# Optimization experiments

Measured on AMD Instinct MI355X. Metric: run time of the kernel, lower is better.

## Reference

```python
import jax, jax.numpy as jnp
import numpy as np

B, IN_DIM, MEM = 8192, 4096, 256
MIN_TS, MAX_TS, EPS = 0.1, 10.0, 1e-6
LN_EPS = 1e-5


def setup_inputs() -> dict:
    key = jax.random.key(0)
    ks = jax.random.split(key, 10)
    std = 0.02
    d_in = MEM + IN_DIM  # 4352
    return {
        "x": jax.random.normal(ks[0], (B, IN_DIM), jnp.float32),
        "h": jax.random.normal(ks[1], (B, MEM), jnp.float32),
        # memory_target: Linear(d_in, 2*MEM) -> LN -> GELU -> Linear(2*MEM, MEM)
        "W1": std * jax.random.normal(ks[2], (d_in, 2 * MEM), jnp.float32),
        "b1": jnp.zeros((2 * MEM,), jnp.float32),
        "g1": jnp.ones((2 * MEM,), jnp.float32),
        "be1": jnp.zeros((2 * MEM,), jnp.float32),
        "W2": std * jax.random.normal(ks[3], (2 * MEM, MEM), jnp.float32),
        "b2": jnp.zeros((MEM,), jnp.float32),
        # decay_gate: Linear(d_in, MEM) -> sigmoid
        "Wd": std * jax.random.normal(ks[4], (d_in, MEM), jnp.float32),
        "bd": jnp.zeros((MEM,), jnp.float32),
        # input_gate: Linear(d_in, MEM) -> sigmoid
        "Wu": std * jax.random.normal(ks[5], (d_in, MEM), jnp.float32),
        "bu": jnp.zeros((MEM,), jnp.float32),
    }


def _layernorm(t, g, b):
    mu = jnp.mean(t, axis=-1, keepdims=True)
    var = jnp.mean(jnp.square(t - mu), axis=-1, keepdims=True)
    return (t - mu) * jax.lax.rsqrt(var + LN_EPS) * g + b


def reference(x, h, W1, b1, g1, be1, W2, b2, Wd, bd, Wu, bu):
    combined = jnp.concatenate([h, x], axis=-1)  # [B, MEM+IN_DIM]
    # memory_target branch: Linear -> LayerNorm -> GELU (exact) -> Linear -> tanh
    t = _layernorm(combined @ W1 + b1, g1, be1)
    t = jax.nn.gelu(t, approximate=False)
    h_candidate = jnp.tanh(t @ W2 + b2)  # [B, MEM]
    # gates
    decay = jax.nn.sigmoid(combined @ Wd + bd)
    update = jax.nn.sigmoid(combined @ Wu + bu)
    decay = MIN_TS + (MAX_TS - MIN_TS) * decay + EPS
    new_h = (1.0 - update) * (h / decay) + update * h_candidate
    # normalize_memory: rescale new_h to old h's L2 norm
    h_norm = jnp.maximum(jnp.linalg.norm(h, axis=-1, keepdims=True), EPS)
    nh_norm = jnp.maximum(jnp.linalg.norm(new_h, axis=-1, keepdims=True), 1e-12)
    new_h = new_h / nh_norm * h_norm
    return new_h
```

## Files before the change

### kernel.cpp

```cpp
#include <hip/hip_runtime.h>
#include <stdint.h>

typedef unsigned short u16;

#define B_ROWS 8192
#define IN_DIM 4096
#define MEM 256
#define D_IN 4352
#define N1 1024
#define K2 512
#define LN_EPS 1e-5f

typedef __attribute__((ext_vector_type(4))) float f32x4;
typedef __attribute__((ext_vector_type(4))) uint32_t u32x4;
typedef __attribute__((ext_vector_type(4))) unsigned short u16x4;
typedef __attribute__((ext_vector_type(8))) short bf16x8;

#define AS1(p) ((__attribute__((address_space(1))) void*)(p))
#define AS3(p) ((__attribute__((address_space(3))) void*)(p))

__device__ __forceinline__ float bf2f(u16 u) {
  union { uint32_t u; float f; } c; c.u = ((uint32_t)u) << 16; return c.f;
}
__device__ __forceinline__ u16 f2bf(float f) {
  union { float f; uint32_t u; } c; c.f = f;
  uint32_t r = (c.u + 0x7fffu + ((c.u >> 16) & 1u)) >> 16;
  return (u16)r;
}
__device__ __forceinline__ uint32_t fbits(float f) {
  union { float f; uint32_t u; } c; c.f = f; return c.u;
}
__device__ __forceinline__ uint32_t pack_trunc(float a, float b) {
  return (fbits(b) & 0xFFFF0000u) | (fbits(a) >> 16);
}

__global__ __launch_bounds__(256)
void transpose_cast_fused(const float* __restrict__ W1, const float* __restrict__ Wd,
                          const float* __restrict__ Wu, u16* __restrict__ WT) {
  __shared__ u16 tile[64][68];
  int n0 = blockIdx.x * 64, k0 = blockIdx.y * 64;
  const float* src; int srcN, ns0;
  if (n0 < 512)      { src = W1; srcN = 512; ns0 = n0; }
  else if (n0 < 768) { src = Wd; srcN = 256; ns0 = n0 - 512; }
  else               { src = Wu; srcN = 256; ns0 = n0 - 768; }
  int t = threadIdx.x;
  int rr = t >> 4;
  int c4 = (t & 15) * 4;
#pragma unroll
  for (int i = 0; i < 4; i++) {
    int k = i * 16 + rr;
    f32x4 v = *(const f32x4*)&src[(size_t)(k0 + k) * srcN + ns0 + c4];
    tile[c4 + 0][k] = f2bf(v[0]);
    tile[c4 + 1][k] = f2bf(v[1]);
    tile[c4 + 2][k] = f2bf(v[2]);
    tile[c4 + 3][k] = f2bf(v[3]);
  }
  __syncthreads();
#pragma unroll
  for (int i = 0; i < 4; i++) {
    int n = i * 16 + rr;
    u16x4 w;
    w.x = tile[n][c4 + 0];
    w.y = tile[n][c4 + 1];
    w.z = tile[n][c4 + 2];
    w.w = tile[n][c4 + 3];
    *(u16x4*)&WT[(size_t)(n0 + n) * D_IN + k0 + c4] = w;
  }
}

__global__ void transpose_cast(const float* __restrict__ src, u16* __restrict__ dst,
                               int K, int N) {
  __shared__ u16 tile[32][34];
  int n0 = blockIdx.x * 32, k0 = blockIdx.y * 32;
  int tx = threadIdx.x, ty = threadIdx.y;
#pragma unroll
  for (int i = 0; i < 4; i++)
    tile[ty + i * 8][tx] = f2bf(src[(size_t)(k0 + ty + i * 8) * N + n0 + tx]);
  __syncthreads();
#pragma unroll
  for (int i = 0; i < 4; i++)
    dst[(size_t)(n0 + ty + i * 8) * K + k0 + tx] = tile[tx][ty + i * 8];
}

__global__ __launch_bounds__(256, 2)
void gemm1_kernel(const float* __restrict__ x, const float* __restrict__ h,
                  const u16* __restrict__ WT, u16* __restrict__ G) {
  __shared__ __attribute__((aligned(16))) u16 As[128 * 64];
  __shared__ __attribute__((aligned(16))) u16 Bs[128 * 64];
  const int t = threadIdx.x;
  const int lane = t & 63, wave = t >> 6;
  const int bx = blockIdx.x >> 6;
  const int by = blockIdx.x & 63;
  const int row0 = by * 128, col0 = bx * 128;
  const int q = lane >> 4, mrow = lane & 15;
  const int wm = wave >> 1, wn = wave & 1;

  int ar[4], ac[4];
#pragma unroll
  for (int j = 0; j < 4; j++) {
    int idx = j * 256 + t;
    int r = idx >> 3;
    ar[j] = r;
    ac[j] = (idx & 7) ^ (r & 7);
  }

  f32x4 acc[4][4] = {};

  for (int k0 = 0; k0 < D_IN; k0 += 64) {
#pragma unroll
    for (int j = 0; j < 4; j++) {
      const u16* gp = WT + (size_t)(col0 + ar[j]) * D_IN + k0 + ac[j] * 8;
      __builtin_amdgcn_global_load_lds(AS1(gp), AS3(&Bs[(j * 256 + t) * 8]), 16, 0, 0);
    }
#pragma unroll
    for (int j = 0; j < 4; j++) {
      int k = k0 + ac[j] * 8;
      const float* gp = (k < MEM) ? (h + (size_t)(row0 + ar[j]) * MEM + k)
                                  : (x + (size_t)(row0 + ar[j]) * IN_DIM + (k - MEM));
      f32x4 v0 = *(const f32x4*)gp;
      f32x4 v1 = *(const f32x4*)(gp + 4);
      u32x4 w;
      w.x = pack_trunc(v0[0], v0[1]);
      w.y = pack_trunc(v0[2], v0[3]);
      w.z = pack_trunc(v1[0], v1[1]);
      w.w = pack_trunc(v1[2], v1[3]);
      *(u32x4*)&As[(j * 256 + t) * 8] = w;
    }
    __syncthreads();
#pragma unroll
    for (int kk = 0; kk < 2; kk++) {
      bf16x8 a[4], b[4];
#pragma unroll
      for (int mt = 0; mt < 4; mt++) {
        int row = wm * 64 + mt * 16 + mrow;
        int p = (kk * 4 + q) ^ (mrow & 7);
        a[mt] = *(const bf16x8*)&As[row * 64 + p * 8];
      }
#pragma unroll
      for (int nt = 0; nt < 4; nt++) {
        int row = wn * 64 + nt * 16 + mrow;
        int p = (kk * 4 + q) ^ (mrow & 7);
        b[nt] = *(const bf16x8*)&Bs[row * 64 + p * 8];
      }
#pragma unroll
      for (int mt = 0; mt < 4; mt++) {
#pragma unroll
        for (int nt = 0; nt < 4; nt++) {
          acc[mt][nt] = __builtin_amdgcn_mfma_f32_16x16x32_bf16(a[mt], b[nt], acc[mt][nt], 0, 0, 0);
        }
      }
    }
    __syncthreads();
  }
#pragma unroll
  for (int mt = 0; mt < 4; mt++) {
#pragma unroll
    for (int nt = 0; nt < 4; nt++) {
#pragma unroll
      for (int i = 0; i < 4; i++) {
        int row = row0 + wm * 64 + mt * 16 + q * 4 + i;
        int col = col0 + wn * 64 + nt * 16 + mrow;
        G[(size_t)row * N1 + col] = f2bf(acc[mt][nt][i]);
      }
    }
  }
}

__global__ __launch_bounds__(256)
void ln_gelu_kernel(u16* __restrict__ G, const float* __restrict__ b1,
                    const float* __restrict__ g1, const float* __restrict__ be1) {
  int r = blockIdx.x;
  int t = threadIdx.x;
  u16* row = G + (size_t)r * N1;
  uint32_t w = *(const uint32_t*)&row[2 * t];
  float z0 = bf2f((u16)(w & 0xffff)) + b1[2 * t];
  float z1 = bf2f((u16)(w >> 16)) + b1[2 * t + 1];
  float s = z0 + z1, ss = z0 * z0 + z1 * z1;
#pragma unroll
  for (int m = 32; m >= 1; m >>= 1) {
    s += __shfl_xor(s, m, 64);
    ss += __shfl_xor(ss, m, 64);
  }
  __shared__ float rs[4], rss[4];
  int lane = t & 63, wave = t >> 6;
  if (lane == 0) { rs[wave] = s; rss[wave] = ss; }
  __syncthreads();
  float S = rs[0] + rs[1] + rs[2] + rs[3];
  float SS = rss[0] + rss[1] + rss[2] + rss[3];
  float mu = S * (1.0f / 512.0f);
  float var = SS * (1.0f / 512.0f) - mu * mu;
  float rstd = rsqrtf(var + LN_EPS);
  float y0 = (z0 - mu) * rstd * g1[2 * t] + be1[2 * t];
  float y1 = (z1 - mu) * rstd * g1[2 * t + 1] + be1[2 * t + 1];
  float o0 = 0.5f * y0 * (1.0f + erff(y0 * 0.7071067811865475f));
  float o1 = 0.5f * y1 * (1.0f + erff(y1 * 0.7071067811865475f));
  *(uint32_t*)&row[2 * t] = ((uint32_t)f2bf(o1) << 16) | f2bf(o0);
}

__global__ __launch_bounds__(256, 2)
void gemm2_epi_kernel(const u16* __restrict__ G, const u16* __restrict__ W2T,
                      const float* __restrict__ h,
                      const float* __restrict__ b2, const float* __restrict__ bd,
                      const float* __restrict__ bu, float* __restrict__ out) {
  __shared__ __attribute__((aligned(16))) u16 As[32 * 64];
  __shared__ __attribute__((aligned(16))) u16 Bs[256 * 64];
  __shared__ float red_nh[32][4], red_h[32][4], scl[32];
  const int t = threadIdx.x, lane = t & 63, wave = t >> 6;
  const int q = lane >> 4, mrow = lane & 15;
  const int r0 = blockIdx.x * 32;

  const int arA = t >> 3;
  const int acA = (t & 7) ^ (arA & 7);
  int brB[8], bcB[8];
#pragma unroll
  for (int j = 0; j < 8; j++) {
    int idx = j * 256 + t;
    brB[j] = idx >> 3;
    bcB[j] = (idx & 7) ^ (brB[j] & 7);
  }
  f32x4 acc[2][4] = {};
  for (int k0 = 0; k0 < K2; k0 += 64) {
    __builtin_amdgcn_global_load_lds(AS1(G + (size_t)(r0 + arA) * N1 + k0 + acA * 8),
                                     AS3(&As[t * 8]), 16, 0, 0);
#pragma unroll
    for (int j = 0; j < 8; j++) {
      __builtin_amdgcn_global_load_lds(AS1(W2T + (size_t)brB[j] * K2 + k0 + bcB[j] * 8),
                                       AS3(&Bs[(j * 256 + t) * 8]), 16, 0, 0);
    }
    __syncthreads();
#pragma unroll
    for (int kk = 0; kk < 2; kk++) {
      bf16x8 a[2], b[4];
#pragma unroll
      for (int mt = 0; mt < 2; mt++) {
        int row = mt * 16 + mrow;
        int p = (kk * 4 + q) ^ (row & 7);
        a[mt] = *(const bf16x8*)&As[row * 64 + p * 8];
      }
#pragma unroll
      for (int nt = 0; nt < 4; nt++) {
        int row = wave * 64 + nt * 16 + mrow;
        int p = (kk * 4 + q) ^ (row & 7);
        b[nt] = *(const bf16x8*)&Bs[row * 64 + p * 8];
      }
#pragma unroll
      for (int mt = 0; mt < 2; mt++) {
#pragma unroll
        for (int nt = 0; nt < 4; nt++) {
          acc[mt][nt] = __builtin_amdgcn_mfma_f32_16x16x32_bf16(a[mt], b[nt], acc[mt][nt], 0, 0, 0);
        }
      }
    }
    __syncthreads();
  }
  float snh[2][4], shh[2][4];
#pragma unroll
  for (int mt = 0; mt < 2; mt++) {
#pragma unroll
    for (int i = 0; i < 4; i++) {
      int r = mt * 16 + q * 4 + i;
      size_t grow = (size_t)(r0 + r);
      float a_nh = 0.f, a_h = 0.f;
#pragma unroll
      for (int nt = 0; nt < 4; nt++) {
        int c = wave * 64 + nt * 16 + mrow;
        float hc = tanhf(acc[mt][nt][i] + b2[c]);
        float zd = bf2f(G[grow * N1 + 512 + c]) + bd[c];
        float zu = bf2f(G[grow * N1 + 768 + c]) + bu[c];
        float dec = 0.1f + 9.9f / (1.0f + expf(-zd)) + 1e-6f;
        float u = 1.0f / (1.0f + expf(-zu));
        float hv = h[grow * MEM + c];
        float nh = (1.0f - u) * (hv / dec) + u * hc;
        acc[mt][nt][i] = nh;
        a_nh += nh * nh;
        a_h += hv * hv;
      }
      snh[mt][i] = a_nh;
      shh[mt][i] = a_h;
    }
  }
#pragma unroll
  for (int m = 1; m <= 8; m <<= 1) {
#pragma unroll
    for (int mt = 0; mt < 2; mt++) {
#pragma unroll
      for (int i = 0; i < 4; i++) {
        snh[mt][i] += __shfl_xor(snh[mt][i], m, 64);
        shh[mt][i] += __shfl_xor(shh[mt][i], m, 64);
      }
    }
  }
  if (mrow == 0) {
#pragma unroll
    for (int mt = 0; mt < 2; mt++) {
#pragma unroll
      for (int i = 0; i < 4; i++) {
        int r = mt * 16 + q * 4 + i;
        red_nh[r][wave] = snh[mt][i];
        red_h[r][wave] = shh[mt][i];
      }
    }
  }
  __syncthreads();
  if (t < 32) {
    float tn = red_nh[t][0] + red_nh[t][1] + red_nh[t][2] + red_nh[t][3];
    float th = red_h[t][0] + red_h[t][1] + red_h[t][2] + red_h[t][3];
    float hn = fmaxf(sqrtf(th), 1e-6f);
    float nn = fmaxf(sqrtf(tn), 1e-12f);
    scl[t] = hn / nn;
  }
  __syncthreads();
#pragma unroll
  for (int mt = 0; mt < 2; mt++) {
#pragma unroll
    for (int i = 0; i < 4; i++) {
      int r = mt * 16 + q * 4 + i;
      size_t grow = (size_t)(r0 + r);
      float sc = scl[r];
#pragma unroll
      for (int nt = 0; nt < 4; nt++) {
        int c = wave * 64 + nt * 16 + mrow;
        out[grow * MEM + c] = acc[mt][nt][i] * sc;
      }
    }
  }
}

extern "C" void kernel_launch(void* const* d_in, const int* in_sizes, int n_in,
                              void* d_out, int out_size, void* d_ws, size_t ws_size,
                              hipStream_t stream) {
  const float* x   = (const float*)d_in[0];
  const float* h   = (const float*)d_in[1];
  const float* W1  = (const float*)d_in[2];
  const float* b1  = (const float*)d_in[3];
  const float* g1  = (const float*)d_in[4];
  const float* be1 = (const float*)d_in[5];
  const float* W2  = (const float*)d_in[6];
  const float* b2  = (const float*)d_in[7];
  const float* Wd  = (const float*)d_in[8];
  const float* bd  = (const float*)d_in[9];
  const float* Wu  = (const float*)d_in[10];
  const float* bu  = (const float*)d_in[11];
  float* out = (float*)d_out;

  char* ws = (char*)d_ws;
  u16* WT  = (u16*)(ws);
  u16* W2T = (u16*)(ws + 8912896);
  u16* G   = (u16*)(ws + 9175040);

  transpose_cast_fused<<<dim3(N1 / 64, D_IN / 64), 256, 0, stream>>>(W1, Wd, Wu, WT);
  transpose_cast<<<dim3(256 / 32, 512 / 32), dim3(32, 8), 0, stream>>>(W2, W2T, 512, 256);

  gemm1_kernel<<<512, 256, 0, stream>>>(x, h, WT, G);
  ln_gelu_kernel<<<B_ROWS, 256, 0, stream>>>(G, b1, g1, be1);
  gemm2_epi_kernel<<<B_ROWS / 32, 256, 0, stream>>>(G, W2T, h, b2, bd, bu, out);
}
```

Measured before the change: 413.7 us.

## Split gemm1 K dimension in two with partial buffers summed downstream

Splits the first GEMM's K loop into two halves, launched as twice as many blocks, each writing a separate bf16 partial buffer. The LayerNorm/GELU and gemm2 epilogue kernels add the two partials before applying biases. The occupancy hint for gemm1 rises to 4 blocks per CU to raise parallelism and latency hiding. In exchange it adds an extra partial-buffer write and read, an extra bf16 rounding of each partial, and risks register spills under the tighter launch bound. The path is used only when the workspace is large enough.

```diff
diff --git a/kernel.cpp b/kernel.cpp
--- a/kernel.cpp
+++ b/kernel.cpp
@@ -82,15 +82,19 @@
     dst[(size_t)(n0 + ty + i * 8) * K + k0 + tx] = tile[tx][ty + i * 8];
 }
 
-__global__ __launch_bounds__(256, 2)
+__global__ __launch_bounds__(256, 4)
 void gemm1_kernel(const float* __restrict__ x, const float* __restrict__ h,
-                  const u16* __restrict__ WT, u16* __restrict__ G) {
+                  const u16* __restrict__ WT, u16* __restrict__ G0,
+                  u16* __restrict__ G1, int klen) {
   __shared__ __attribute__((aligned(16))) u16 As[128 * 64];
   __shared__ __attribute__((aligned(16))) u16 Bs[128 * 64];
   const int t = threadIdx.x;
   const int lane = t & 63, wave = t >> 6;
-  const int bx = blockIdx.x >> 6;
   const int by = blockIdx.x & 63;
+  const int bx = (blockIdx.x >> 6) & 7;
+  const int part = blockIdx.x >> 9;
+  const int kbase = part * klen;
+  u16* __restrict__ Gout = part ? G1 : G0;
   const int row0 = by * 128, col0 = bx * 128;
   const int q = lane >> 4, mrow = lane & 15;
   const int wm = wave >> 1, wn = wave & 1;
@@ -106,7 +110,7 @@
 
   f32x4 acc[4][4] = {};
 
-  for (int k0 = 0; k0 < D_IN; k0 += 64) {
+  for (int k0 = kbase; k0 < kbase + klen; k0 += 64) {
 #pragma unroll
     for (int j = 0; j < 4; j++) {
       const u16* gp = WT + (size_t)(col0 + ar[j]) * D_IN + k0 + ac[j] * 8;
@@ -160,21 +164,29 @@
       for (int i = 0; i < 4; i++) {
         int row = row0 + wm * 64 + mt * 16 + q * 4 + i;
         int col = col0 + wn * 64 + nt * 16 + mrow;
-        G[(size_t)row * N1 + col] = f2bf(acc[mt][nt][i]);
+        Gout[(size_t)row * N1 + col] = f2bf(acc[mt][nt][i]);
       }
     }
   }
 }
 
 __global__ __launch_bounds__(256)
-void ln_gelu_kernel(u16* __restrict__ G, const float* __restrict__ b1,
-                    const float* __restrict__ g1, const float* __restrict__ be1) {
+void ln_gelu_kernel(u16* __restrict__ G0, const u16* __restrict__ G1,
+                    const float* __restrict__ b1, const float* __restrict__ g1,
+                    const float* __restrict__ be1, int nparts) {
   int r = blockIdx.x;
   int t = threadIdx.x;
-  u16* row = G + (size_t)r * N1;
+  u16* row = G0 + (size_t)r * N1;
   uint32_t w = *(const uint32_t*)&row[2 * t];
-  float z0 = bf2f((u16)(w & 0xffff)) + b1[2 * t];
-  float z1 = bf2f((u16)(w >> 16)) + b1[2 * t + 1];
+  float z0 = bf2f((u16)(w & 0xffff));
+  float z1 = bf2f((u16)(w >> 16));
+  if (nparts == 2) {
+    uint32_t w1 = *(const uint32_t*)&G1[(size_t)r * N1 + 2 * t];
+    z0 += bf2f((u16)(w1 & 0xffff));
+    z1 += bf2f((u16)(w1 >> 16));
+  }
+  z0 += b1[2 * t];
+  z1 += b1[2 * t + 1];
   float s = z0 + z1, ss = z0 * z0 + z1 * z1;
 #pragma unroll
   for (int m = 32; m >= 1; m >>= 1) {
@@ -198,10 +210,11 @@
 }
 
 __global__ __launch_bounds__(256, 2)
-void gemm2_epi_kernel(const u16* __restrict__ G, const u16* __restrict__ W2T,
-                      const float* __restrict__ h,
+void gemm2_epi_kernel(const u16* __restrict__ G0, const u16* __restrict__ G1,
+                      const u16* __restrict__ W2T, const float* __restrict__ h,
                       const float* __restrict__ b2, const float* __restrict__ bd,
-                      const float* __restrict__ bu, float* __restrict__ out) {
+                      const float* __restrict__ bu, float* __restrict__ out,
+                      int nparts) {
   __shared__ __attribute__((aligned(16))) u16 As[32 * 64];
   __shared__ __attribute__((aligned(16))) u16 Bs[256 * 64];
   __shared__ float red_nh[32][4], red_h[32][4], scl[32];
@@ -220,7 +233,7 @@
   }
   f32x4 acc[2][4] = {};
   for (int k0 = 0; k0 < K2; k0 += 64) {
-    __builtin_amdgcn_global_load_lds(AS1(G + (size_t)(r0 + arA) * N1 + k0 + acA * 8),
+    __builtin_amdgcn_global_load_lds(AS1(G0 + (size_t)(r0 + arA) * N1 + k0 + acA * 8),
                                      AS3(&As[t * 8]), 16, 0, 0);
 #pragma unroll
     for (int j = 0; j < 8; j++) {
@@ -265,8 +278,14 @@
       for (int nt = 0; nt < 4; nt++) {
         int c = wave * 64 + nt * 16 + mrow;
         float hc = tanhf(acc[mt][nt][i] + b2[c]);
-        float zd = bf2f(G[grow * N1 + 512 + c]) + bd[c];
-        float zu = bf2f(G[grow * N1 + 768 + c]) + bu[c];
+        float zd = bf2f(G0[grow * N1 + 512 + c]);
+        float zu = bf2f(G0[grow * N1 + 768 + c]);
+        if (nparts == 2) {
+          zd += bf2f(G1[grow * N1 + 512 + c]);
+          zu += bf2f(G1[grow * N1 + 768 + c]);
+        }
+        zd += bd[c];
+        zu += bu[c];
         float dec = 0.1f + 9.9f / (1.0f + expf(-zd)) + 1e-6f;
         float u = 1.0f / (1.0f + expf(-zu));
         float hv = h[grow * MEM + c];
@@ -346,12 +365,16 @@
   char* ws = (char*)d_ws;
   u16* WT  = (u16*)(ws);
   u16* W2T = (u16*)(ws + 8912896);
-  u16* G   = (u16*)(ws + 9175040);
+  u16* G0  = (u16*)(ws + 9175040);
+  u16* G1  = (u16*)(ws + 25952256);
+
+  const int nparts = (ws_size >= 42729472u) ? 2 : 1;
+  const int klen = D_IN / nparts;
 
   transpose_cast_fused<<<dim3(N1 / 64, D_IN / 64), 256, 0, stream>>>(W1, Wd, Wu, WT);
   transpose_cast<<<dim3(256 / 32, 512 / 32), dim3(32, 8), 0, stream>>>(W2, W2T, 512, 256);
 
-  gemm1_kernel<<<512, 256, 0, stream>>>(x, h, WT, G);
-  ln_gelu_kernel<<<B_ROWS, 256, 0, stream>>>(G, b1, g1, be1);
-  gemm2_epi_kernel<<<B_ROWS / 32, 256, 0, stream>>>(G, W2T, h, b2, bd, bu, out);
-}
+  gemm1_kernel<<<512 * nparts, 256, 0, stream>>>(x, h, WT, G0, G1, klen);
+  ln_gelu_kernel<<<B_ROWS, 256, 0, stream>>>(G0, G1, b1, g1, be1, nparts);
+  gemm2_epi_kernel<<<B_ROWS / 32, 256, 0, stream>>>(G0, G1, W2T, h, b2, bd, bu, out, nparts);
+}
```

Result: faster. 388.1 us (-6.2%).
